# Kernel tuning notes

Measured on AMD Instinct MI355X. Metric: run time of the kernel, lower is better.

The kernel has to match this reference:

```python
import jax, jax.numpy as jnp
import numpy as np

D = 512            # model size
H = 8              # num_heads
HD = D // H        # head_size = 64
WIN = 7            # num_keys (payload tokens per window)
QNB = 5            # query_nb for 'mean' aggregation
SCALE = D ** -0.5  # NOTE: torch module scales by size**-0.5, not head_size**-0.5
EPS = 1e-5


def setup_inputs() -> dict:
    key = jax.random.key(0)
    ks = jax.random.split(key, 12)
    B, M = 8, 4096
    w = lambda i: jax.random.normal(ks[i], (D, D), jnp.float32) * 0.02
    return {
        "k": jax.random.normal(ks[0], (B, M, D), jnp.float32),
        "v": jax.random.normal(ks[1], (B, M, D), jnp.float32),
        "q": jax.random.normal(ks[2], (B, M, D), jnp.float32),
        "query_len": 3584,
        "Wk": w(3), "bk": jnp.zeros((D,), jnp.float32),
        "Wv": w(4), "bv": jnp.zeros((D,), jnp.float32),
        "Wq": w(5), "bq": jnp.zeros((D,), jnp.float32),
        "ln_g": jnp.ones((D,), jnp.float32), "ln_b": jnp.zeros((D,), jnp.float32),
        "Wpq": w(6), "bpq": jnp.zeros((D,), jnp.float32),
        "Wpk": w(7), "bpk": jnp.zeros((D,), jnp.float32),
        "Wo": w(8), "bo": jnp.zeros((D,), jnp.float32),
    }


def reference(k, v, q, query_len, Wk, bk, Wv, bv, Wq, bq, ln_g, ln_b, Wpq, bpq, Wpk, bpk, Wo, bo):
    B, M, _ = k.shape
    win_num = -(-query_len // WIN)     # ceil
    per_win = M // win_num

    k = k @ Wk + bk
    v = v @ Wv + bv
    q = q @ Wq + bq

    # 'mean' query aggregation: AvgPool1d(kernel=QNB, stride=1, pad=QNB//2),
    # count_include_pad=True => always divide by QNB (zero-padded)
    qp = jnp.pad(q, ((0, 0), (QNB // 2, QNB // 2), (0, 0)))
    q = sum(qp[:, j:j + M] for j in range(QNB)) / QNB

    # ---- stage 1: DSA (local attention inside each window of per_win tokens)
    resh = lambda x: x.reshape(B, win_num, per_win, H, HD).transpose(0, 1, 3, 2, 4)
    dq, dk, dv = resh(q), resh(k), resh(v)                       # [B,W,H,p,hd]
    attn = jax.nn.softmax(jnp.einsum('bwhqd,bwhkd->bwhqk', dq, dk) * SCALE, axis=-1)
    out = jnp.einsum('bwhqk,bwhkd->bwhqd', attn, dv)
    out = out.transpose(0, 1, 3, 2, 4).reshape(B, win_num, per_win, D)

    win_tok = out[:, :, 0, :]          # [B, W, D] window summary tokens
    attn_x = out[:, :, 1:, :]

    # LayerNorm + exact GELU on window tokens
    mu = win_tok.mean(-1, keepdims=True)
    var = ((win_tok - mu) ** 2).mean(-1, keepdims=True)
    win_tok = (win_tok - mu) / jnp.sqrt(var + EPS) * ln_g + ln_b
    win_tok = jax.nn.gelu(win_tok, approximate=False)

    # ---- stage 2: PSA (attention over window summary tokens)
    pq = (win_tok @ Wpq + bpq).reshape(B, win_num, H, HD).transpose(0, 2, 1, 3)  # [B,H,W,hd]
    pk = (win_tok @ Wpk + bpk).reshape(B, win_num, H, HD).transpose(0, 2, 1, 3)
    pv = attn_x.reshape(B, win_num, WIN, H, HD).transpose(0, 3, 1, 2, 4)
    pv = pv.reshape(B, H, win_num, WIN * HD)

    pattn = jax.nn.softmax(jnp.einsum('bhqd,bhkd->bhqk', pq, pk) * SCALE, axis=-1)
    pout = jnp.einsum('bhqk,bhkd->bhqd', pattn, pv)
    pout = pout.transpose(0, 2, 1, 3).reshape(B, win_num, H, WIN, HD)
    pout = pout.transpose(0, 1, 3, 2, 4).reshape(B, win_num, WIN, D)

    out = (pout + attn_x).reshape(B, win_num * WIN, D)[:, :query_len, :]
    return out @ Wo + bo
```

## Files before the change

kernel.cpp:

```cpp
#include <hip/hip_runtime.h>
#include <hip/hip_bf16.h>
#include <math.h>

#define SCALE_ 0.04419417382415922f
#define EPS_  1e-5f

typedef unsigned short u16;
typedef __attribute__((ext_vector_type(8))) short     bf16x8;
typedef __attribute__((ext_vector_type(4))) float     f32x4;
typedef __attribute__((ext_vector_type(8))) unsigned short u16x8;
typedef __attribute__((ext_vector_type(4))) unsigned short u16x4;

__device__ __forceinline__ u16 f2b(float f) {
  union { float f; unsigned int u; } x; x.f = f;
  unsigned int u = x.u;
  return (u16)((u + 0x7FFFu + ((u >> 16) & 1u)) >> 16);
}
__device__ __forceinline__ float b2f(u16 h) {
  union { unsigned int u; float f; } x; x.u = ((unsigned int)h) << 16;
  return x.f;
}
__device__ __forceinline__ void gload_lds16(const void* g, void* l) {
  __builtin_amdgcn_global_load_lds(
      (const __attribute__((address_space(1))) void*)g,
      (__attribute__((address_space(3))) void*)l, 16, 0, 0);
}

__global__ __launch_bounds__(256) void wconv(
    const float* W0, const float* W1, const float* W2,
    const float* W3, const float* W4, const float* W5, u16* wt)
{
  const float* W;
  switch (blockIdx.z) {
    case 0: W = W0; break; case 1: W = W1; break; case 2: W = W2; break;
    case 3: W = W3; break; case 4: W = W4; break; default: W = W5; break;
  }
  u16* Wt = wt + (size_t)blockIdx.z * 262144;
  const int k0 = blockIdx.x * 64, n0 = blockIdx.y * 64;
  __shared__ float T[64][68];
  const int tid = threadIdx.x;
#pragma unroll
  for (int it = 0; it < 4; ++it) {
    int L = it * 256 + tid;
    int r = L >> 4, cg = L & 15;
    float4 v = *reinterpret_cast<const float4*>(W + (size_t)(k0 + r) * 512 + n0 + cg * 4);
    T[r][cg * 4 + 0] = v.x; T[r][cg * 4 + 1] = v.y;
    T[r][cg * 4 + 2] = v.z; T[r][cg * 4 + 3] = v.w;
  }
  __syncthreads();
#pragma unroll
  for (int it = 0; it < 2; ++it) {
    int L = it * 256 + tid;
    int rn = L >> 3, kg = L & 7;
    u16x8 o;
#pragma unroll
    for (int e = 0; e < 8; ++e) o[e] = f2b(T[kg * 8 + e][rn]);
    *(u16x8*)(Wt + (size_t)(n0 + rn) * 512 + k0 + kg * 8) = o;
  }
}

__global__ __launch_bounds__(512) void gemm_proj(
    const float* A0, const u16* Bt0, const float* bi0, u16* C0,
    const float* A1, const u16* Bt1, const float* bi1, u16* C1,
    const float* A2, const u16* Bt2, const float* bi2, u16* C2)
{
  const float *A, *bias; const u16* Bt; u16* C;
  if (blockIdx.z == 0)      { A = A0; Bt = Bt0; bias = bi0; C = C0; }
  else if (blockIdx.z == 1) { A = A1; Bt = Bt1; bias = bi1; C = C1; }
  else                      { A = A2; Bt = Bt2; bias = bi2; C = C2; }

  __shared__ u16 As[8192];
  __shared__ u16 Bs[32768];
  const int tid = threadIdx.x;
  const int lane = tid & 63, wid = tid >> 6;
  const int wr = wid >> 2, wcn = wid & 3;
  const int l15 = lane & 15, lh = lane >> 4, l7 = lane & 7;
  const int m0 = blockIdx.x * 128;

  const f32x4 fz = {0.f, 0.f, 0.f, 0.f};
  f32x4 acc[4][8];
#pragma unroll
  for (int m = 0; m < 4; ++m)
#pragma unroll
    for (int n = 0; n < 8; ++n) acc[m][n] = fz;

  int aoff[2], boff[2];
#pragma unroll
  for (int kh = 0; kh < 2; ++kh) {
    int slot = ((kh * 4 + lh) ^ l7) << 4;
    aoff[kh] = (wr * 64 + l15) * 128 + slot;
    boff[kh] = (wcn * 128 + l15) * 128 + slot;
  }

  for (int k0 = 0; k0 < 512; k0 += 64) {
    __syncthreads();
#pragma unroll
    for (int it = 0; it < 8; ++it) {
      int L = it * 512 + tid;
      int r = L >> 3, s = L & 7;
      int c = s ^ (r & 7);
      gload_lds16(Bt + (size_t)r * 512 + k0 + c * 8,
                  (char*)Bs + (it * 512 + wid * 64) * 16);
    }
    float4 xa[2], xb[2];
#pragma unroll
    for (int it = 0; it < 2; ++it) {
      int L = it * 512 + tid;
      int r = L >> 3, s = L & 7;
      int c = s ^ (r & 7);
      const float* ga = A + (size_t)(m0 + r) * 512 + k0 + c * 8;
      xa[it] = *reinterpret_cast<const float4*>(ga);
      xb[it] = *reinterpret_cast<const float4*>(ga + 4);
    }
#pragma unroll
    for (int it = 0; it < 2; ++it) {
      int L = it * 512 + tid;
      u16x8 o;
      o[0] = f2b(xa[it].x); o[1] = f2b(xa[it].y);
      o[2] = f2b(xa[it].z); o[3] = f2b(xa[it].w);
      o[4] = f2b(xb[it].x); o[5] = f2b(xb[it].y);
      o[6] = f2b(xb[it].z); o[7] = f2b(xb[it].w);
      *(u16x8*)((char*)As + L * 16) = o;
    }
    __syncthreads();
#pragma unroll
    for (int kh = 0; kh < 2; ++kh) {
      bf16x8 af[4], bfr[8];
#pragma unroll
      for (int m = 0; m < 4; ++m)
        af[m] = *(const bf16x8*)((const char*)As + aoff[kh] + m * 2048);
#pragma unroll
      for (int n = 0; n < 8; ++n)
        bfr[n] = *(const bf16x8*)((const char*)Bs + boff[kh] + n * 2048);
#pragma unroll
      for (int m = 0; m < 4; ++m)
#pragma unroll
        for (int n = 0; n < 8; ++n)
          acc[m][n] = __builtin_amdgcn_mfma_f32_16x16x32_bf16(af[m], bfr[n], acc[m][n], 0, 0, 0);
    }
  }

  const int gn0 = wcn * 128 + l15;
  float bv[8];
#pragma unroll
  for (int n = 0; n < 8; ++n) bv[n] = bias[gn0 + n * 16];
#pragma unroll
  for (int m = 0; m < 4; ++m)
#pragma unroll
    for (int reg = 0; reg < 4; ++reg) {
      int gm = m0 + wr * 64 + m * 16 + lh * 4 + reg;
#pragma unroll
      for (int n = 0; n < 8; ++n)
        C[(size_t)gm * 512 + gn0 + n * 16] = f2b(acc[m][n][reg] + bv[n]);
    }
}

__global__ __launch_bounds__(512) void gemm_out(
    const u16* __restrict__ A, const u16* __restrict__ Bt,
    const float* __restrict__ bias, float* __restrict__ C)
{
  __shared__ u16 As[2][4096];
  __shared__ u16 Bs[2][16384];
  const int tid = threadIdx.x;
  const int lane = tid & 63, wid = tid >> 6;
  const int wr = wid >> 2, wcn = wid & 3;
  const int l15 = lane & 15, lh = lane >> 4;
  const int sx = (l15 >> 1) & 3;
  const int m0 = blockIdx.x * 128;
  const int rr = tid >> 2, sp = tid & 3;
  const int ssw = sp ^ ((rr >> 1) & 3);

  const f32x4 fz = {0.f, 0.f, 0.f, 0.f};
  f32x4 acc[4][8];
#pragma unroll
  for (int m = 0; m < 4; ++m)
#pragma unroll
    for (int n = 0; n < 8; ++n) acc[m][n] = fz;

  const int aoff0 = (wr * 64 + l15) * 64 + ((lh ^ sx) << 4);
  const int boff0 = (wcn * 128 + l15) * 64 + ((lh ^ sx) << 4);

  {
#pragma unroll
    for (int it = 0; it < 4; ++it)
      gload_lds16(Bt + (size_t)(it * 128 + rr) * 512 + ssw * 8,
                  (char*)Bs[0] + (it * 512 + wid * 64) * 16);
    gload_lds16(A + (size_t)(m0 + rr) * 512 + ssw * 8,
                (char*)As[0] + (wid * 64) * 16);
  }
  __syncthreads();

#pragma unroll 2
  for (int t = 0; t < 16; ++t) {
    const int cur = t & 1, nxt = cur ^ 1;
    if (t < 15) {
      const int k0 = (t + 1) * 32;
#pragma unroll
      for (int it = 0; it < 4; ++it)
        gload_lds16(Bt + (size_t)(it * 128 + rr) * 512 + k0 + ssw * 8,
                    (char*)Bs[nxt] + (it * 512 + wid * 64) * 16);
      gload_lds16(A + (size_t)(m0 + rr) * 512 + k0 + ssw * 8,
                  (char*)As[nxt] + (wid * 64) * 16);
    }
    bf16x8 af[4], bfr[8];
#pragma unroll
    for (int m = 0; m < 4; ++m)
      af[m] = *(const bf16x8*)((const char*)As[cur] + aoff0 + m * 1024);
#pragma unroll
    for (int n = 0; n < 8; ++n)
      bfr[n] = *(const bf16x8*)((const char*)Bs[cur] + boff0 + n * 1024);
#pragma unroll
    for (int m = 0; m < 4; ++m)
#pragma unroll
      for (int n = 0; n < 8; ++n)
        acc[m][n] = __builtin_amdgcn_mfma_f32_16x16x32_bf16(af[m], bfr[n], acc[m][n], 0, 0, 0);
    __syncthreads();
  }

  const int gn0 = wcn * 128 + l15;
  float bv[8];
#pragma unroll
  for (int n = 0; n < 8; ++n) bv[n] = bias[gn0 + n * 16];
#pragma unroll
  for (int m = 0; m < 4; ++m)
#pragma unroll
    for (int reg = 0; reg < 4; ++reg) {
      int gm = m0 + wr * 64 + m * 16 + lh * 4 + reg;
#pragma unroll
      for (int n = 0; n < 8; ++n)
        C[(size_t)gm * 512 + gn0 + n * 16] = acc[m][n][reg] + bv[n];
    }
}

__global__ __launch_bounds__(256) void gemm_pp(
    const u16* __restrict__ A,
    const u16* __restrict__ Bt0, const float* __restrict__ bi0, u16* __restrict__ C0,
    const u16* __restrict__ Bt1, const float* __restrict__ bi1, u16* __restrict__ C1)
{
  const u16* Bt; const float* bias; u16* C;
  if (blockIdx.z == 0) { Bt = Bt0; bias = bi0; C = C0; }
  else                 { Bt = Bt1; bias = bi1; C = C1; }

  __shared__ u16 As[8192];
  __shared__ u16 Bs[8192];
  const int tid = threadIdx.x;
  const int lane = tid & 63, wid = tid >> 6;
  const int wr = wid >> 1, wc = wid & 1;
  const int l15 = lane & 15, lh = lane >> 4, l7 = lane & 7;
  const int m0 = blockIdx.x * 128, n0 = blockIdx.y * 128;

  const f32x4 fz = {0.f, 0.f, 0.f, 0.f};
  f32x4 acc[4][4];
#pragma unroll
  for (int m = 0; m < 4; ++m)
#pragma unroll
    for (int n = 0; n < 4; ++n) acc[m][n] = fz;

  int aoff[2], boff[2];
#pragma unroll
  for (int kh = 0; kh < 2; ++kh) {
    int slot = ((kh * 4 + lh) ^ l7) << 4;
    aoff[kh] = (wr * 64 + l15) * 128 + slot;
    boff[kh] = (wc * 64 + l15) * 128 + slot;
  }

  for (int k0 = 0; k0 < 512; k0 += 64) {
    __syncthreads();
#pragma unroll
    for (int it = 0; it < 4; ++it) {
      int L = it * 256 + tid;
      int r = L >> 3, s = L & 7;
      int c = s ^ (r & 7);
      gload_lds16(A  + (size_t)(m0 + r) * 512 + k0 + c * 8,
                  (char*)As + (it * 256 + wid * 64) * 16);
      gload_lds16(Bt + (size_t)(n0 + r) * 512 + k0 + c * 8,
                  (char*)Bs + (it * 256 + wid * 64) * 16);
    }
    __syncthreads();
#pragma unroll
    for (int kh = 0; kh < 2; ++kh) {
      bf16x8 af[4], bfr[4];
#pragma unroll
      for (int m = 0; m < 4; ++m)
        af[m] = *(const bf16x8*)((const char*)As + aoff[kh] + m * 2048);
#pragma unroll
      for (int n = 0; n < 4; ++n)
        bfr[n] = *(const bf16x8*)((const char*)Bs + boff[kh] + n * 2048);
#pragma unroll
      for (int m = 0; m < 4; ++m)
#pragma unroll
        for (int n = 0; n < 4; ++n)
          acc[m][n] = __builtin_amdgcn_mfma_f32_16x16x32_bf16(af[m], bfr[n], acc[m][n], 0, 0, 0);
    }
  }

  const int gn0 = n0 + wc * 64 + l15;
  float bv[4];
#pragma unroll
  for (int n = 0; n < 4; ++n) bv[n] = bias[gn0 + n * 16];
#pragma unroll
  for (int m = 0; m < 4; ++m)
#pragma unroll
    for (int reg = 0; reg < 4; ++reg) {
      int gm = m0 + wr * 64 + m * 16 + lh * 4 + reg;
#pragma unroll
      for (int n = 0; n < 4; ++n)
        C[(size_t)gm * 512 + gn0 + n * 16] = f2b(acc[m][n][reg] + bv[n]);
    }
}

__global__ __launch_bounds__(512) void pattn(
    const u16* __restrict__ pq, const u16* __restrict__ pk,
    const u16* __restrict__ pvT, const u16* __restrict__ attn,
    u16* __restrict__ X2)
{
  __shared__ u16 Aq[8192];
  __shared__ u16 Bk[4096];
  __shared__ u16 Pl[8192];
  __shared__ u16 Vt[28672];
  __shared__ float rsl[128];

  const int tid = threadIdx.x;
  const int lane = tid & 63, wid = tid >> 6;
  const int wr = wid >> 2, wcn = wid & 3;
  const int l15 = lane & 15, lh = lane >> 4, l7 = lane & 7;
  const int bh = blockIdx.x & 63;
  const int wq0 = (blockIdx.x >> 6) * 128;
  const int b = bh >> 3, h = bh & 7;

  const f32x4 fz = {0.f, 0.f, 0.f, 0.f};
  f32x4 acc[4][7];
#pragma unroll
  for (int m = 0; m < 4; ++m)
#pragma unroll
    for (int n = 0; n < 7; ++n) acc[m][n] = fz;
  float rs4[4] = {0.f, 0.f, 0.f, 0.f};

#pragma unroll
  for (int it = 0; it < 2; ++it) {
    int L = it * 512 + tid;
    int r = L >> 3, s = L & 7;
    int c = s ^ (r & 7);
    gload_lds16(pq + ((size_t)b * 512 + wq0 + r) * 512 + h * 64 + c * 8,
                (char*)Aq + L * 16);
  }

  int slotk[2];
#pragma unroll
  for (int kh = 0; kh < 2; ++kh) slotk[kh] = ((kh * 4 + lh) ^ l7) << 4;

  for (int wk0 = 0; wk0 < 512; wk0 += 64) {
    {
      int L = tid;
      int r = L >> 3, s = L & 7;
      int c = s ^ (r & 7);
      gload_lds16(pk + ((size_t)b * 512 + wk0 + r) * 512 + h * 64 + c * 8,
                  (char*)Bk + L * 16);
    }
#pragma unroll
    for (int it = 0; it < 7; ++it) {
      int L = it * 512 + tid;
      int r = L >> 3, s = L & 7;
      int c = s ^ (r & 7);
      gload_lds16(pvT + ((size_t)bh * 448 + r) * 512 + wk0 + c * 8,
                  (char*)Vt + L * 16);
    }
    __syncthreads();

    f32x4 pacc[4];
#pragma unroll
    for (int n = 0; n < 4; ++n) pacc[n] = fz;
#pragma unroll
    for (int kh = 0; kh < 2; ++kh) {
      bf16x8 af = *(const bf16x8*)((const char*)Aq + (wid * 16 + l15) * 128 + slotk[kh]);
#pragma unroll
      for (int n = 0; n < 4; ++n) {
        bf16x8 bfr = *(const bf16x8*)((const char*)Bk + (n * 16 + l15) * 128 + slotk[kh]);
        pacc[n] = __builtin_amdgcn_mfma_f32_16x16x32_bf16(af, bfr, pacc[n], 0, 0, 0);
      }
    }
#pragma unroll
    for (int n = 0; n < 4; ++n)
#pragma unroll
      for (int reg = 0; reg < 4; ++reg) {
        float e = expf(pacc[n][reg] * SCALE_);
        rs4[reg] += e;
        int prow = wid * 16 + lh * 4 + reg;
        int pcol = n * 16 + l15;
        int phys = (pcol >> 3) ^ (prow & 7);
        *(u16*)((char*)Pl + prow * 128 + phys * 16 + (pcol & 7) * 2) = f2b(e);
      }
    __syncthreads();

#pragma unroll
    for (int kh = 0; kh < 2; ++kh) {
      bf16x8 af[4], bfr[7];
#pragma unroll
      for (int m = 0; m < 4; ++m)
        af[m] = *(const bf16x8*)((const char*)Pl + (wr * 64 + m * 16 + l15) * 128 + slotk[kh]);
#pragma unroll
      for (int n = 0; n < 7; ++n)
        bfr[n] = *(const bf16x8*)((const char*)Vt + (wcn * 112 + n * 16 + l15) * 128 + slotk[kh]);
#pragma unroll
      for (int m = 0; m < 4; ++m)
#pragma unroll
        for (int n = 0; n < 7; ++n)
          acc[m][n] = __builtin_amdgcn_mfma_f32_16x16x32_bf16(af[m], bfr[n], acc[m][n], 0, 0, 0);
    }
    __syncthreads();
  }

#pragma unroll
  for (int reg = 0; reg < 4; ++reg) {
    float v = rs4[reg];
    v += __shfl_xor(v, 1);
    v += __shfl_xor(v, 2);
    v += __shfl_xor(v, 4);
    v += __shfl_xor(v, 8);
    if (l15 == 0) rsl[wid * 16 + lh * 4 + reg] = v;
  }
  __syncthreads();

#pragma unroll
  for (int m = 0; m < 4; ++m)
#pragma unroll
    for (int reg = 0; reg < 4; ++reg) {
      int lrow = wr * 64 + m * 16 + lh * 4 + reg;
      int gm = wq0 + lrow;
      float ri = 1.0f / rsl[lrow];
#pragma unroll
      for (int n = 0; n < 7; ++n) {
        int nd = wcn * 112 + n * 16 + l15;
        int nt = nd >> 6, d = nd & 63;
        float res = b2f(attn[((size_t)b * 4096 + gm * 8 + nt + 1) * 512 + h * 64 + d]);
        X2[((size_t)b * 3584 + gm * 7 + nt) * 512 + h * 64 + d] =
            f2b(acc[m][n][reg] * ri + res);
      }
    }
}

__global__ __launch_bounds__(64) void attn_win(
    const u16* kp, const u16* vp, const u16* qp0, u16* attn)
{
  const int h = blockIdx.x, w = blockIdx.y, b = blockIdx.z;
  const int t = threadIdx.x;
  __shared__ float ks[8][68], vs[8][68], qr[12][68], qs[8][68], Ps[8][9];
  const size_t base = ((size_t)b * 4096 + (size_t)w * 8) * 512 + h * 64;

  {
    int i = t >> 3, dg = t & 7;
    u16x8 kv = *(const u16x8*)(kp + base + (size_t)i * 512 + dg * 8);
    u16x8 vv = *(const u16x8*)(vp + base + (size_t)i * 512 + dg * 8);
#pragma unroll
    for (int e = 0; e < 8; ++e) {
      ks[i][dg * 8 + e] = b2f(kv[e]);
      vs[i][dg * 8 + e] = b2f(vv[e]);
    }
  }
#pragma unroll
  for (int l = 0; l < 2; ++l) {
    int L = t + l * 64;
    if (L < 96) {
      int i = L >> 3, dg = L & 7;
      int m = w * 8 - 2 + i;
      if (m >= 0 && m < 4096) {
        u16x8 qv = *(const u16x8*)(qp0 + ((size_t)b * 4096 + m) * 512 + h * 64 + dg * 8);
#pragma unroll
        for (int e = 0; e < 8; ++e) qr[i][dg * 8 + e] = b2f(qv[e]);
      } else {
#pragma unroll
        for (int e = 0; e < 8; ++e) qr[i][dg * 8 + e] = 0.0f;
      }
    }
  }
  __syncthreads();
#pragma unroll
  for (int j = 0; j < 8; ++j)
    qs[j][t] = 0.2f * (qr[j][t] + qr[j + 1][t] + qr[j + 2][t] + qr[j + 3][t] + qr[j + 4][t]);
  __syncthreads();

  const int qi = t >> 3, kj = t & 7;
  float s = 0.0f;
#pragma unroll
  for (int d = 0; d < 64; ++d) s = fmaf(qs[qi][d], ks[kj][d], s);
  s *= SCALE_;
  float mx = s;
  mx = fmaxf(mx, __shfl_xor(mx, 1));
  mx = fmaxf(mx, __shfl_xor(mx, 2));
  mx = fmaxf(mx, __shfl_xor(mx, 4));
  float e = expf(s - mx);
  float sum = e;
  sum += __shfl_xor(sum, 1);
  sum += __shfl_xor(sum, 2);
  sum += __shfl_xor(sum, 4);
  Ps[qi][kj] = e / sum;
  __syncthreads();

  float o[8];
#pragma unroll
  for (int c = 0; c < 8; ++c) o[c] = 0.0f;
#pragma unroll
  for (int tt = 0; tt < 8; ++tt) {
    float pw = Ps[qi][tt];
#pragma unroll
    for (int c = 0; c < 8; ++c) o[c] = fmaf(pw, vs[tt][kj * 8 + c], o[c]);
  }
  u16x8 ov;
#pragma unroll
  for (int c = 0; c < 8; ++c) ov[c] = f2b(o[c]);
  *(u16x8*)(attn + base + (size_t)qi * 512 + kj * 8) = ov;
}

__global__ __launch_bounds__(256) void pvt_build(const u16* attn, u16* pvT)
{
  const int bh = blockIdx.x;
  const int b = bh >> 3, h = bh & 7;
  const int w0 = blockIdx.y * 32;
  __shared__ u16 TL[448 * 40];
  const int tid = threadIdx.x;
#pragma unroll
  for (int it = 0; it < 8; ++it) {
    int L = it * 256 + tid;
    int dg = L & 7, r = L >> 3;
    int w2l = r >> 3, tt = r & 7;
    if (tt < 7) {
      int m = 8 * (w0 + w2l) + tt + 1;
      u16x8 v = *(const u16x8*)(attn + ((size_t)b * 4096 + m) * 512 + h * 64 + dg * 8);
#pragma unroll
      for (int e = 0; e < 8; ++e)
        TL[(tt * 64 + dg * 8 + e) * 40 + w2l] = v[e];
    }
  }
  __syncthreads();
#pragma unroll
  for (int it = 0; it < 7; ++it) {
    int L = it * 256 + tid;
    int n = L >> 2, seg = L & 3;
    u16x8 v = *(const u16x8*)(&TL[n * 40 + seg * 8]);
    *(u16x8*)(pvT + ((size_t)bh * 448 + n) * 512 + w0 + seg * 8) = v;
  }
}

__global__ __launch_bounds__(64) void ln_gelu(
    const u16* attn, const float* g, const float* be, u16* wt)
{
  const int r = blockIdx.x;
  const int b = r >> 9, w = r & 511;
  const int t = threadIdx.x;
  const u16* x = attn + (((size_t)b * 4096) + (size_t)w * 8) * 512;

  u16x8 v = *(const u16x8*)(x + t * 8);
  float xv[8];
  float s1 = 0.f, s2 = 0.f;
#pragma unroll
  for (int e = 0; e < 8; ++e) {
    xv[e] = b2f(v[e]);
    s1 += xv[e]; s2 += xv[e] * xv[e];
  }
#pragma unroll
  for (int off = 1; off < 64; off <<= 1) {
    s1 += __shfl_xor(s1, off);
    s2 += __shfl_xor(s2, off);
  }
  const float mu  = s1 * (1.0f / 512.0f);
  const float var = s2 * (1.0f / 512.0f) - mu * mu;
  const float inv = 1.0f / sqrtf(var + EPS_);

  const int d0 = t * 8;
  float4 g0 = *reinterpret_cast<const float4*>(g + d0);
  float4 g1 = *reinterpret_cast<const float4*>(g + d0 + 4);
  float4 b0 = *reinterpret_cast<const float4*>(be + d0);
  float4 b1 = *reinterpret_cast<const float4*>(be + d0 + 4);
  float gv[8] = {g0.x, g0.y, g0.z, g0.w, g1.x, g1.y, g1.z, g1.w};
  float bvv[8] = {b0.x, b0.y, b0.z, b0.w, b1.x, b1.y, b1.z, b1.w};
  const float k2 = 0.70710678118654752f;
  u16x8 ov;
#pragma unroll
  for (int e = 0; e < 8; ++e) {
    float y = (xv[e] - mu) * inv * gv[e] + bvv[e];
    ov[e] = f2b(0.5f * y * (1.0f + erff(y * k2)));
  }
  *(u16x8*)(wt + (size_t)r * 512 + d0) = ov;
}

extern "C" void kernel_launch(void* const* d_in, const int* in_sizes, int n_in,
                              void* d_out, int out_size, void* d_ws, size_t ws_size,
                              hipStream_t stream)
{
  const float* k_in = (const float*)d_in[0];
  const float* v_in = (const float*)d_in[1];
  const float* q_in = (const float*)d_in[2];
  const float* Wk  = (const float*)d_in[4];
  const float* bk  = (const float*)d_in[5];
  const float* Wv  = (const float*)d_in[6];
  const float* bv  = (const float*)d_in[7];
  const float* Wq  = (const float*)d_in[8];
  const float* bq  = (const float*)d_in[9];
  const float* lng = (const float*)d_in[10];
  const float* lnb = (const float*)d_in[11];
  const float* Wpq = (const float*)d_in[12];
  const float* bpq = (const float*)d_in[13];
  const float* Wpk = (const float*)d_in[14];
  const float* bpk = (const float*)d_in[15];
  const float* Wo  = (const float*)d_in[16];
  const float* bo  = (const float*)d_in[17];
  float* out = (float*)d_out;

  char* ws = (char*)d_ws;
  const size_t MB = 1024 * 1024;
  u16* wtb  = (u16*)(ws);
  u16* kp   = (u16*)(ws + 16 * MB);
  u16* vp   = (u16*)(ws + 52 * MB);
  u16* qp0  = (u16*)(ws + 88 * MB);
  u16* attn = (u16*)(ws + 124 * MB);
  u16*   wt    = (u16*)(ws + 16 * MB);
  u16*   pq    = (u16*)(ws + 20 * MB);
  u16*   pk    = (u16*)(ws + 28 * MB);
  u16*   pvT   = (u16*)(ws + 76 * MB);
  u16*   X2    = (u16*)(ws + 160 * MB);

  u16* Wkt  = wtb;
  u16* Wvt  = wtb + 1 * 262144;
  u16* Wqt  = wtb + 2 * 262144;
  u16* Wpqt = wtb + 3 * 262144;
  u16* Wpkt = wtb + 4 * 262144;
  u16* Wot  = wtb + 5 * 262144;

  wconv<<<dim3(8, 8, 6), 256, 0, stream>>>(Wk, Wv, Wq, Wpq, Wpk, Wo, wtb);

  gemm_proj<<<dim3(256, 1, 3), 512, 0, stream>>>(
      k_in, Wkt, bk, kp,
      v_in, Wvt, bv, vp,
      q_in, Wqt, bq, qp0);

  attn_win<<<dim3(8, 512, 8), 64, 0, stream>>>(kp, vp, qp0, attn);
  pvt_build<<<dim3(64, 16), 256, 0, stream>>>(attn, pvT);
  ln_gelu<<<4096, 64, 0, stream>>>(attn, lng, lnb, wt);

  gemm_pp<<<dim3(32, 4, 2), 256, 0, stream>>>(
      wt, Wpqt, bpq, pq, Wpkt, bpk, pk);

  pattn<<<256, 512, 0, stream>>>(pq, pk, pvT, attn, X2);

  gemm_out<<<dim3(224, 1, 1), 512, 0, stream>>>(X2, Wot, bo, out);
}
```

Baseline: 256.5 us.

## Retile projection and output GEMMs to 64x256 tiles with 256-thread blocks

Both the input projection GEMM and the output GEMM move from 128x512 tiles on 512-thread blocks to 64x256 tiles on 256-thread blocks. This quadruples the number of blocks, so the 256 CUs are filled better, and halves the shared memory per block. The output GEMM also drops its double-buffered 32-wide K pipeline for a single-buffered 64-wide K loop that uses the same XOR swizzle as the projection kernel. The cost is that each A and B tile is reloaded more often across blocks, and the output GEMM no longer overlaps its loads with compute.

```diff
diff --git a/kernel.cpp b/kernel.cpp
--- a/kernel.cpp
+++ b/kernel.cpp
@@ -59,53 +59,53 @@
   }
 }
 
-__global__ __launch_bounds__(512) void gemm_proj(
+__global__ __launch_bounds__(256) void gemm_proj(
     const float* A0, const u16* Bt0, const float* bi0, u16* C0,
     const float* A1, const u16* Bt1, const float* bi1, u16* C1,
     const float* A2, const u16* Bt2, const float* bi2, u16* C2)
 {
   const float *A, *bias; const u16* Bt; u16* C;
-  if (blockIdx.z == 0)      { A = A0; Bt = Bt0; bias = bi0; C = C0; }
-  else if (blockIdx.z == 1) { A = A1; Bt = Bt1; bias = bi1; C = C1; }
+  if (blockIdx.y == 0)      { A = A0; Bt = Bt0; bias = bi0; C = C0; }
+  else if (blockIdx.y == 1) { A = A1; Bt = Bt1; bias = bi1; C = C1; }
   else                      { A = A2; Bt = Bt2; bias = bi2; C = C2; }
 
-  __shared__ u16 As[8192];
-  __shared__ u16 Bs[32768];
+  __shared__ u16 As[4096];
+  __shared__ u16 Bs[16384];
   const int tid = threadIdx.x;
   const int lane = tid & 63, wid = tid >> 6;
-  const int wr = wid >> 2, wcn = wid & 3;
   const int l15 = lane & 15, lh = lane >> 4, l7 = lane & 7;
-  const int m0 = blockIdx.x * 128;
+  const int m0 = (blockIdx.x >> 1) * 64;
+  const int n0 = (blockIdx.x & 1) * 256;
 
   const f32x4 fz = {0.f, 0.f, 0.f, 0.f};
-  f32x4 acc[4][8];
-#pragma unroll
-  for (int m = 0; m < 4; ++m)
-#pragma unroll
-    for (int n = 0; n < 8; ++n) acc[m][n] = fz;
+  f32x4 acc[4][4];
+#pragma unroll
+  for (int m = 0; m < 4; ++m)
+#pragma unroll
+    for (int n = 0; n < 4; ++n) acc[m][n] = fz;
 
   int aoff[2], boff[2];
 #pragma unroll
   for (int kh = 0; kh < 2; ++kh) {
     int slot = ((kh * 4 + lh) ^ l7) << 4;
-    aoff[kh] = (wr * 64 + l15) * 128 + slot;
-    boff[kh] = (wcn * 128 + l15) * 128 + slot;
+    aoff[kh] = l15 * 128 + slot;
+    boff[kh] = (wid * 64 + l15) * 128 + slot;
   }
 
   for (int k0 = 0; k0 < 512; k0 += 64) {
     __syncthreads();
 #pragma unroll
     for (int it = 0; it < 8; ++it) {
-      int L = it * 512 + tid;
+      int L = it * 256 + tid;
       int r = L >> 3, s = L & 7;
       int c = s ^ (r & 7);
-      gload_lds16(Bt + (size_t)r * 512 + k0 + c * 8,
-                  (char*)Bs + (it * 512 + wid * 64) * 16);
+      gload_lds16(Bt + (size_t)(n0 + r) * 512 + k0 + c * 8,
+                  (char*)Bs + L * 16);
     }
     float4 xa[2], xb[2];
 #pragma unroll
     for (int it = 0; it < 2; ++it) {
-      int L = it * 512 + tid;
+      int L = it * 256 + tid;
       int r = L >> 3, s = L & 7;
       int c = s ^ (r & 7);
       const float* ga = A + (size_t)(m0 + r) * 512 + k0 + c * 8;
@@ -114,7 +114,7 @@
     }
 #pragma unroll
     for (int it = 0; it < 2; ++it) {
-      int L = it * 512 + tid;
+      int L = it * 256 + tid;
       u16x8 o;
       o[0] = f2b(xa[it].x); o[1] = f2b(xa[it].y);
       o[2] = f2b(xa[it].z); o[3] = f2b(xa[it].w);
@@ -125,109 +125,110 @@
     __syncthreads();
 #pragma unroll
     for (int kh = 0; kh < 2; ++kh) {
-      bf16x8 af[4], bfr[8];
+      bf16x8 af[4], bfr[4];
 #pragma unroll
       for (int m = 0; m < 4; ++m)
         af[m] = *(const bf16x8*)((const char*)As + aoff[kh] + m * 2048);
 #pragma unroll
-      for (int n = 0; n < 8; ++n)
+      for (int n = 0; n < 4; ++n)
         bfr[n] = *(const bf16x8*)((const char*)Bs + boff[kh] + n * 2048);
 #pragma unroll
       for (int m = 0; m < 4; ++m)
 #pragma unroll
-        for (int n = 0; n < 8; ++n)
+        for (int n = 0; n < 4; ++n)
           acc[m][n] = __builtin_amdgcn_mfma_f32_16x16x32_bf16(af[m], bfr[n], acc[m][n], 0, 0, 0);
     }
   }
 
-  const int gn0 = wcn * 128 + l15;
-  float bv[8];
-#pragma unroll
-  for (int n = 0; n < 8; ++n) bv[n] = bias[gn0 + n * 16];
+  const int gn0 = n0 + wid * 64 + l15;
+  float bv[4];
+#pragma unroll
+  for (int n = 0; n < 4; ++n) bv[n] = bias[gn0 + n * 16];
 #pragma unroll
   for (int m = 0; m < 4; ++m)
 #pragma unroll
     for (int reg = 0; reg < 4; ++reg) {
-      int gm = m0 + wr * 64 + m * 16 + lh * 4 + reg;
-#pragma unroll
-      for (int n = 0; n < 8; ++n)
+      int gm = m0 + m * 16 + lh * 4 + reg;
+#pragma unroll
+      for (int n = 0; n < 4; ++n)
         C[(size_t)gm * 512 + gn0 + n * 16] = f2b(acc[m][n][reg] + bv[n]);
     }
 }
 
-__global__ __launch_bounds__(512) void gemm_out(
+__global__ __launch_bounds__(256) void gemm_out(
     const u16* __restrict__ A, const u16* __restrict__ Bt,
     const float* __restrict__ bias, float* __restrict__ C)
 {
-  __shared__ u16 As[2][4096];
-  __shared__ u16 Bs[2][16384];
+  __shared__ u16 As[4096];
+  __shared__ u16 Bs[16384];
   const int tid = threadIdx.x;
   const int lane = tid & 63, wid = tid >> 6;
-  const int wr = wid >> 2, wcn = wid & 3;
-  const int l15 = lane & 15, lh = lane >> 4;
-  const int sx = (l15 >> 1) & 3;
-  const int m0 = blockIdx.x * 128;
-  const int rr = tid >> 2, sp = tid & 3;
-  const int ssw = sp ^ ((rr >> 1) & 3);
+  const int l15 = lane & 15, lh = lane >> 4, l7 = lane & 7;
+  const int m0 = (blockIdx.x >> 1) * 64;
+  const int n0 = (blockIdx.x & 1) * 256;
 
   const f32x4 fz = {0.f, 0.f, 0.f, 0.f};
-  f32x4 acc[4][8];
-#pragma unroll
-  for (int m = 0; m < 4; ++m)
-#pragma unroll
-    for (int n = 0; n < 8; ++n) acc[m][n] = fz;
-
-  const int aoff0 = (wr * 64 + l15) * 64 + ((lh ^ sx) << 4);
-  const int boff0 = (wcn * 128 + l15) * 64 + ((lh ^ sx) << 4);
-
-  {
-#pragma unroll
-    for (int it = 0; it < 4; ++it)
-      gload_lds16(Bt + (size_t)(it * 128 + rr) * 512 + ssw * 8,
-                  (char*)Bs[0] + (it * 512 + wid * 64) * 16);
-    gload_lds16(A + (size_t)(m0 + rr) * 512 + ssw * 8,
-                (char*)As[0] + (wid * 64) * 16);
-  }
-  __syncthreads();
-
-#pragma unroll 2
-  for (int t = 0; t < 16; ++t) {
-    const int cur = t & 1, nxt = cur ^ 1;
-    if (t < 15) {
-      const int k0 = (t + 1) * 32;
-#pragma unroll
-      for (int it = 0; it < 4; ++it)
-        gload_lds16(Bt + (size_t)(it * 128 + rr) * 512 + k0 + ssw * 8,
-                    (char*)Bs[nxt] + (it * 512 + wid * 64) * 16);
-      gload_lds16(A + (size_t)(m0 + rr) * 512 + k0 + ssw * 8,
-                  (char*)As[nxt] + (wid * 64) * 16);
-    }
-    bf16x8 af[4], bfr[8];
-#pragma unroll
-    for (int m = 0; m < 4; ++m)
-      af[m] = *(const bf16x8*)((const char*)As[cur] + aoff0 + m * 1024);
-#pragma unroll
-    for (int n = 0; n < 8; ++n)
-      bfr[n] = *(const bf16x8*)((const char*)Bs[cur] + boff0 + n * 1024);
-#pragma unroll
-    for (int m = 0; m < 4; ++m)
-#pragma unroll
-      for (int n = 0; n < 8; ++n)
-        acc[m][n] = __builtin_amdgcn_mfma_f32_16x16x32_bf16(af[m], bfr[n], acc[m][n], 0, 0, 0);
-    __syncthreads();
-  }
-
-  const int gn0 = wcn * 128 + l15;
-  float bv[8];
-#pragma unroll
-  for (int n = 0; n < 8; ++n) bv[n] = bias[gn0 + n * 16];
+  f32x4 acc[4][4];
+#pragma unroll
+  for (int m = 0; m < 4; ++m)
+#pragma unroll
+    for (int n = 0; n < 4; ++n) acc[m][n] = fz;
+
+  int aoff[2], boff[2];
+#pragma unroll
+  for (int kh = 0; kh < 2; ++kh) {
+    int slot = ((kh * 4 + lh) ^ l7) << 4;
+    aoff[kh] = l15 * 128 + slot;
+    boff[kh] = (wid * 64 + l15) * 128 + slot;
+  }
+
+  for (int k0 = 0; k0 < 512; k0 += 64) {
+    __syncthreads();
+#pragma unroll
+    for (int it = 0; it < 8; ++it) {
+      int L = it * 256 + tid;
+      int r = L >> 3, s = L & 7;
+      int c = s ^ (r & 7);
+      gload_lds16(Bt + (size_t)(n0 + r) * 512 + k0 + c * 8,
+                  (char*)Bs + L * 16);
+    }
+#pragma unroll
+    for (int it = 0; it < 2; ++it) {
+      int L = it * 256 + tid;
+      int r = L >> 3, s = L & 7;
+      int c = s ^ (r & 7);
+      gload_lds16(A + (size_t)(m0 + r) * 512 + k0 + c * 8,
+                  (char*)As + L * 16);
+    }
+    __syncthreads();
+#pragma unroll
+    for (int kh = 0; kh < 2; ++kh) {
+      bf16x8 af[4], bfr[4];
+#pragma unroll
+      for (int m = 0; m < 4; ++m)
+        af[m] = *(const bf16x8*)((const char*)As + aoff[kh] + m * 2048);
+#pragma unroll
+      for (int n = 0; n < 4; ++n)
+        bfr[n] = *(const bf16x8*)((const char*)Bs + boff[kh] + n * 2048);
+#pragma unroll
+      for (int m = 0; m < 4; ++m)
+#pragma unroll
+        for (int n = 0; n < 4; ++n)
+          acc[m][n] = __builtin_amdgcn_mfma_f32_16x16x32_bf16(af[m], bfr[n], acc[m][n], 0, 0, 0);
+    }
+  }
+
+  const int gn0 = n0 + wid * 64 + l15;
+  float bv[4];
+#pragma unroll
+  for (int n = 0; n < 4; ++n) bv[n] = bias[gn0 + n * 16];
 #pragma unroll
   for (int m = 0; m < 4; ++m)
 #pragma unroll
     for (int reg = 0; reg < 4; ++reg) {
-      int gm = m0 + wr * 64 + m * 16 + lh * 4 + reg;
-#pragma unroll
-      for (int n = 0; n < 8; ++n)
+      int gm = m0 + m * 16 + lh * 4 + reg;
+#pragma unroll
+      for (int n = 0; n < 4; ++n)
         C[(size_t)gm * 512 + gn0 + n * 16] = acc[m][n][reg] + bv[n];
     }
 }
@@ -628,7 +629,7 @@
 
   wconv<<<dim3(8, 8, 6), 256, 0, stream>>>(Wk, Wv, Wq, Wpq, Wpk, Wo, wtb);
 
-  gemm_proj<<<dim3(256, 1, 3), 512, 0, stream>>>(
+  gemm_proj<<<dim3(1024, 3), 256, 0, stream>>>(
       k_in, Wkt, bk, kp,
       v_in, Wvt, bv, vp,
       q_in, Wqt, bq, qp0);
@@ -642,5 +643,5 @@
 
   pattn<<<256, 512, 0, stream>>>(pq, pk, pvT, attn, X2);
 
-  gemm_out<<<dim3(224, 1, 1), 512, 0, stream>>>(X2, Wot, bo, out);
-}
+  gemm_out<<<896, 256, 0, stream>>>(X2, Wot, bo, out);
+}
```

New measurement: 274.7 us. 1.07x slower.
